# Kernel tuning notes

Hardware: AMD Instinct MI355X
Metric: run time of the kernel (lower is better)

The kernel has to match this reference:

```python
import jax, jax.numpy as jnp
import numpy as np


def _conv1x1(x, w, b):
    # x: [B, Cin, H, W], w: [Cout, Cin], b: [Cout]
    return jnp.einsum('bchw,oc->bohw', x, w) + b[None, :, None, None]


def setup_inputs() -> dict:
    key = jax.random.key(0)
    ks = jax.random.split(key, 9)
    B, C, H, W = 32, 512, 32, 32
    Cout, dn = 512, 512
    s_in = 1.0 / np.sqrt(C)
    s_out = 1.0 / np.sqrt(Cout)
    return {
        'x': jax.random.normal(ks[0], (B, C, H, W), jnp.float32),
        'wA': jax.random.uniform(ks[1], (Cout, C), jnp.float32, -s_in, s_in),
        'bA': jax.random.uniform(ks[2], (Cout,), jnp.float32, -s_in, s_in),
        'wB': jax.random.uniform(ks[3], (dn, C), jnp.float32, -s_in, s_in),
        'bB': jax.random.uniform(ks[4], (dn,), jnp.float32, -s_in, s_in),
        'wV': jax.random.uniform(ks[5], (dn, C), jnp.float32, -s_in, s_in),
        'bV': jax.random.uniform(ks[6], (dn,), jnp.float32, -s_in, s_in),
        'wR': jax.random.uniform(ks[7], (Cout, Cout), jnp.float32, -s_out, s_out),
        'bR': jax.random.uniform(ks[8], (Cout,), jnp.float32, -s_out, s_out),
    }


def reference(x, wA, bA, wB, bB, wV, bV, wR, bR):
    Bsz, C, H, W = x.shape
    Cout = wA.shape[0]
    A = _conv1x1(x, wA, bA).reshape(Bsz, Cout, H * W)          # [B, Cout, N]
    Bm = _conv1x1(x, wB, bB).reshape(Bsz, wB.shape[0], H * W)  # [B, dn, N]
    Vm = _conv1x1(x, wV, bV).reshape(Bsz, wV.shape[0], H * W)  # [B, dn, N]
    attn_maps = jax.nn.softmax(Bm, axis=-1)                    # softmax over spatial
    attn_vectors = jax.nn.softmax(Vm, axis=-1)                 # softmax over spatial
    glob_desc = jnp.einsum('bcn,bdn->bcd', A, attn_maps)       # [B, Cout, dn]
    Z = jnp.einsum('bcd,bdn->bcn', glob_desc, attn_vectors)    # [B, Cout, N]
    Z = Z.reshape(Bsz, Cout, H, W)
    Z = _conv1x1(Z, wR, bR)
    return Z
```

## Files before the change

### kernel.cpp

```cpp
#include <hip/hip_runtime.h>
#include <stdint.h>

typedef unsigned short u16;
typedef __bf16  bf16x8 __attribute__((ext_vector_type(8)));
typedef float   f32x4  __attribute__((ext_vector_type(4)));

__device__ __forceinline__ u16 f2bf(float f) {
    union { float f; unsigned u; } c; c.f = f;
    unsigned r = c.u + 0x7fffu + ((c.u >> 16) & 1u);
    return (u16)(r >> 16);
}
__device__ __forceinline__ float bf2f(u16 b) {
    union { unsigned u; float f; } c; c.u = ((unsigned)b) << 16; return c.f;
}

__device__ __forceinline__ void g2l16(const u16* g, u16* l) {
    __builtin_amdgcn_global_load_lds(
        (__attribute__((address_space(1))) void*)(uintptr_t)g,
        (__attribute__((address_space(3))) void*)(uint32_t)(uintptr_t)l,
        16, 0, 0);
}

template <int TM, bool HAS_BIAS, bool OUT_F32, bool EPI>
__device__ __forceinline__ void gemm_core(
    const u16* __restrict__ Ab, const u16* __restrict__ Bb, void* __restrict__ C,
    const float* __restrict__ bias, int N, int K, long cbase, int m0, int n0,
    const float* __restrict__ svec, const float* __restrict__ wRbA)
{
    constexpr int MI = TM / 32;
    constexpr int NA = TM / 32;
    __shared__ __align__(16) u16 As[TM * 64];
    __shared__ __align__(16) u16 Bs[128 * 64];

    const int t = threadIdx.x;
    const int w = t >> 6, lane = t & 63;
    const int wr = w >> 1, wc = w & 1;

    f32x4 acc[MI][4];
    const f32x4 zero = {0.f, 0.f, 0.f, 0.f};
#pragma unroll
    for (int i = 0; i < MI; ++i)
#pragma unroll
        for (int j = 0; j < 4; ++j) acc[i][j] = zero;

    int  aslot[NA]; long aoff[NA];
#pragma unroll
    for (int i = 0; i < NA; ++i) {
        const int s   = i * 256 + t;
        const int row = s >> 3;
        const int col = ((s & 7) ^ (row & 7)) * 8;
        aslot[i] = s * 8;
        aoff[i]  = (long)(m0 + row) * K + col;
    }
    int  bslot[4]; long boff[4];
#pragma unroll
    for (int i = 0; i < 4; ++i) {
        const int s   = i * 256 + t;
        const int row = s >> 3;
        const int col = ((s & 7) ^ (row & 7)) * 8;
        bslot[i] = s * 8;
        boff[i]  = (long)(n0 + row) * K + col;
    }

    const int fr = lane & 15;
    const int q  = lane >> 4;
    const int o0 = ((q ^ (fr & 7)) * 8);
    const u16* fa = &As[(wr * (TM / 2) + fr) * 64];
    const u16* fb = &Bs[(wc * 64 + fr) * 64];

    for (int k0 = 0; k0 < K; k0 += 64) {
#pragma unroll
        for (int i = 0; i < NA; ++i) g2l16(Ab + aoff[i] + k0, &As[aslot[i]]);
#pragma unroll
        for (int i = 0; i < 4; ++i)  g2l16(Bb + boff[i] + k0, &Bs[bslot[i]]);
        __syncthreads();

#pragma unroll
        for (int kh = 0; kh < 2; ++kh) {
            const int o = o0 ^ (kh * 32);
            bf16x8 af[MI], bv[4];
#pragma unroll
            for (int mi = 0; mi < MI; ++mi) af[mi] = *(const bf16x8*)(fa + mi * 1024 + o);
#pragma unroll
            for (int ni = 0; ni < 4; ++ni)  bv[ni] = *(const bf16x8*)(fb + ni * 1024 + o);
#pragma unroll
            for (int mi = 0; mi < MI; ++mi)
#pragma unroll
                for (int ni = 0; ni < 4; ++ni)
                    acc[mi][ni] = __builtin_amdgcn_mfma_f32_16x16x32_bf16(
                        af[mi], bv[ni], acc[mi][ni], 0, 0, 0);
        }
        __syncthreads();
    }

    const int ccol  = n0 + wc * 64 + fr;
    const int crow0 = m0 + wr * (TM / 2) + (lane >> 4) * 4;
    float se[4];
    if (EPI) {
#pragma unroll
        for (int ni = 0; ni < 4; ++ni) se[ni] = svec[ccol + ni * 16];
    }
#pragma unroll
    for (int mi = 0; mi < MI; ++mi) {
#pragma unroll
        for (int r = 0; r < 4; ++r) {
            const int row = crow0 + mi * 16 + r;
            float add = HAS_BIAS ? bias[row] : 0.f;
            float rk  = EPI ? wRbA[row] : 0.f;
#pragma unroll
            for (int ni = 0; ni < 4; ++ni) {
                float v = acc[mi][ni][r] + add;
                if (EPI) v += rk * se[ni];
                const long idx = cbase + (long)row * N + ccol + ni * 16;
                if (OUT_F32) ((float*)C)[idx] = v;
                else         ((u16*)C)[idx]   = f2bf(v);
            }
        }
    }
}

template <int TM, bool HAS_BIAS, bool OUT_F32>
__global__ __launch_bounds__(256) void gemm_nt(
    const u16* __restrict__ A, const u16* __restrict__ B, void* __restrict__ C,
    const float* __restrict__ bias, int N, int K, long sA, long sB, long sC)
{
    const int bz = blockIdx.z;
    gemm_core<TM, HAS_BIAS, OUT_F32, false>(
        A + (long)bz * sA, B + (long)bz * sB, C, bias, N, K,
        (long)bz * sC, blockIdx.y * TM, blockIdx.x * 128, nullptr, nullptr);
}

template <int TM, bool HAS_BIAS, bool OUT_F32, bool EPI>
__global__ __launch_bounds__(256) void gemm_nt_swz(
    const u16* __restrict__ A, const u16* __restrict__ B, void* __restrict__ C,
    const float* __restrict__ bias, int N, int K, long sA, long sB, long sC,
    int bxn, int bpb, const float* __restrict__ s_all,
    const float* __restrict__ wRbA)
{
    const int blk  = blockIdx.x;
    const int xcd  = blk & 7;
    const int slot = blk >> 3;
    const int b    = xcd + 8 * (slot / bpb);
    const int wi   = slot % bpb;
    const int bx   = wi % bxn;
    const int by   = wi / bxn;
    gemm_core<TM, HAS_BIAS, OUT_F32, EPI>(
        A + (long)b * sA, B + (long)b * sB, C, bias, N, K,
        (long)b * sC, by * TM, bx * 128,
        EPI ? s_all + (long)b * 1024 : nullptr, wRbA);
}

__global__ __launch_bounds__(256) void cast_transpose_x(
    const float* __restrict__ in, u16* __restrict__ out)
{
    __shared__ u16 tile[64][68];
    const int bz = blockIdx.z;
    const float* ip = in  + (long)bz * (512 * 1024);
    u16*         op = out + (long)bz * (1024 * 512);
    const int c0 = blockIdx.x * 64;
    const int r0 = blockIdx.y * 64;
    const int tx = threadIdx.x & 15;
    const int ty = threadIdx.x >> 4;
#pragma unroll
    for (int p = 0; p < 4; ++p) {
        const int row = ty + 16 * p;
        float4 v = *(const float4*)(ip + (long)(r0 + row) * 1024 + c0 + 4 * tx);
        ushort4 o;
        o.x = f2bf(v.x); o.y = f2bf(v.y); o.z = f2bf(v.z); o.w = f2bf(v.w);
        *(ushort4*)&tile[row][4 * tx] = o;
    }
    __syncthreads();
#pragma unroll
    for (int p = 0; p < 4; ++p) {
        const int orow = ty + 16 * p;
        ushort4 o;
        o.x = tile[4 * tx + 0][orow];
        o.y = tile[4 * tx + 1][orow];
        o.z = tile[4 * tx + 2][orow];
        o.w = tile[4 * tx + 3][orow];
        *(ushort4*)&op[(long)(c0 + orow) * 512 + r0 + 4 * tx] = o;
    }
}

__global__ __launch_bounds__(256) void transpose_colsum(
    const u16* __restrict__ in, u16* __restrict__ out, float* __restrict__ s,
    long sIn, long sOut)
{
    __shared__ u16 tile[64][68];
    const int bz = blockIdx.z;
    const u16* ip = in  + (long)bz * sIn;
    u16*       op = out + (long)bz * sOut;
    const int c0 = blockIdx.x * 64;
    const int r0 = blockIdx.y * 64;
    const int t  = threadIdx.x;
    const int tx = t & 15;
    const int ty = t >> 4;
#pragma unroll
    for (int p = 0; p < 4; ++p) {
        const int row = ty + 16 * p;
        ushort4 v = *(const ushort4*)(ip + (long)(r0 + row) * 1024 + c0 + 4 * tx);
        *(ushort4*)&tile[row][4 * tx] = v;
    }
    __syncthreads();
#pragma unroll
    for (int p = 0; p < 4; ++p) {
        const int orow = ty + 16 * p;
        ushort4 o;
        o.x = tile[4 * tx + 0][orow];
        o.y = tile[4 * tx + 1][orow];
        o.z = tile[4 * tx + 2][orow];
        o.w = tile[4 * tx + 3][orow];
        *(ushort4*)&op[(long)(c0 + orow) * 512 + r0 + 4 * tx] = o;
    }
    if (t < 64) {
        float a = 0.f;
#pragma unroll 8
        for (int d = 0; d < 64; ++d) a += bf2f(tile[d][t]);
        atomicAdd(&s[(long)bz * 1024 + c0 + t], a);
    }
}

__global__ __launch_bounds__(256) void cast_weights(
    const float* __restrict__ wA, const float* __restrict__ wB,
    const float* __restrict__ wV, const float* __restrict__ wR,
    const float* __restrict__ bB, const float* __restrict__ bV,
    u16* __restrict__ Wcat, u16* __restrict__ wRb, u16* __restrict__ wAtb,
    float* __restrict__ bcat)
{
    const int tid = blockIdx.x * 256 + threadIdx.x;
    if (tid < 262144) {
        Wcat[262144 + tid] = f2bf(wB[tid]);
    } else if (tid < 524288) {
        Wcat[262144 + tid] = f2bf(wV[tid - 262144]);
    } else if (tid < 786432) {
        wRb[tid - 524288] = f2bf(wR[tid - 524288]);
    } else if (tid < 1048576) {
        const int i = tid - 786432;
        wAtb[(i & 511) * 512 + (i >> 9)] = f2bf(wA[i]);
    } else if (tid < 1048576 + 1536) {
        const int j = tid - 1048576;
        bcat[j] = (j < 512) ? 0.f : (j < 1024) ? bB[j - 512] : bV[j - 1024];
    }
}

__global__ __launch_bounds__(256) void compute_wrba(
    const float* __restrict__ wR, const float* __restrict__ bA,
    float* __restrict__ wRbA)
{
    const int o    = blockIdx.x * 4 + (threadIdx.x >> 6);
    const int lane = threadIdx.x & 63;
    float a = 0.f;
#pragma unroll
    for (int c = lane; c < 512; c += 64) a += wR[o * 512 + c] * bA[c];
#pragma unroll
    for (int off = 32; off > 0; off >>= 1) a += __shfl_down(a, off);
    if (lane == 0) wRbA[o] = a;
}

__global__ __launch_bounds__(256) void softmax_rows(u16* __restrict__ Y)
{
    u16* row = Y + (long)blockIdx.y * (1536 * 1024) + (long)(512 + blockIdx.x) * 1024;
    const int t = threadIdx.x;
    ushort4 u = ((const ushort4*)row)[t];
    float v0 = bf2f(u.x), v1 = bf2f(u.y), v2 = bf2f(u.z), v3 = bf2f(u.w);

    float m = fmaxf(fmaxf(v0, v1), fmaxf(v2, v3));
#pragma unroll
    for (int off = 32; off > 0; off >>= 1) m = fmaxf(m, __shfl_down(m, off));

    __shared__ float smax[4];
    __shared__ float ssum[4];
    const int w = t >> 6, lane = t & 63;
    if (lane == 0) smax[w] = m;
    __syncthreads();
    m = fmaxf(fmaxf(smax[0], smax[1]), fmaxf(smax[2], smax[3]));

    float e0 = __expf(v0 - m), e1 = __expf(v1 - m);
    float e2 = __expf(v2 - m), e3 = __expf(v3 - m);
    float s = e0 + e1 + e2 + e3;
#pragma unroll
    for (int off = 32; off > 0; off >>= 1) s += __shfl_down(s, off);
    if (lane == 0) ssum[w] = s;
    __syncthreads();
    const float inv = 1.0f / (ssum[0] + ssum[1] + ssum[2] + ssum[3]);

    ushort4 o;
    o.x = f2bf(e0 * inv); o.y = f2bf(e1 * inv);
    o.z = f2bf(e2 * inv); o.w = f2bf(e3 * inv);
    ((ushort4*)row)[t] = o;
}

extern "C" void kernel_launch(void* const* d_in, const int* in_sizes, int n_in,
                              void* d_out, int out_size, void* d_ws, size_t ws_size,
                              hipStream_t stream)
{
    (void)in_sizes; (void)n_in; (void)out_size; (void)ws_size;
    const float* x  = (const float*)d_in[0];
    const float* wA = (const float*)d_in[1];
    const float* bA = (const float*)d_in[2];
    const float* wB = (const float*)d_in[3];
    const float* bB = (const float*)d_in[4];
    const float* wV = (const float*)d_in[5];
    const float* bV = (const float*)d_in[6];
    const float* wR = (const float*)d_in[7];
    const float* bR = (const float*)d_in[8];
    float* out = (float*)d_out;

    const int B = 32;
    const long sY = (long)1536 * 1024;

    char* p = (char*)d_ws;
    u16*   Y    = (u16*)p;   p += (long)B * sY * 2;
    u16*   H    = (u16*)p;   p += (long)B * 512 * 512 * 2;
    u16*   Wcat = (u16*)p;   p += (long)1536 * 512 * 2;
    u16*   wRb  = (u16*)p;   p += (long)512 * 512 * 2;
    u16*   wAtb = (u16*)p;   p += (long)512 * 512 * 2;
    float* bcat = (float*)p; p += 1536 * 4;
    float* svec = (float*)p; p += (long)B * 1024 * 4;
    float* wRbA = (float*)p; p += 512 * 4;

    u16* Xt = (u16*)d_out;
    u16* Vt = Y;

    cast_transpose_x<<<dim3(16, 8, B), 256, 0, stream>>>(x, Xt);
    cast_weights<<<dim3(4103), 256, 0, stream>>>(wA, wB, wV, wR, bB, bV,
                                                 Wcat, wRb, wAtb, bcat);
    compute_wrba<<<dim3(128), 256, 0, stream>>>(wR, bA, wRbA);
    hipMemsetAsync(svec, 0, (long)B * 1024 * 4, stream);

    gemm_nt<128, false, false><<<dim3(4, 4, 1), 256, 0, stream>>>(
        wRb, wAtb, Wcat, nullptr, 512, 512, 0, 0, 0);

    gemm_nt<128, true, false><<<dim3(8, 12, B), 256, 0, stream>>>(
        Wcat, Xt, Y, bcat, 1024, 512, 0, (long)1024 * 512, sY);

    softmax_rows<<<dim3(1024, B), 256, 0, stream>>>(Y);

    gemm_nt_swz<128, false, false, false><<<dim3(512), 256, 0, stream>>>(
        Y, Y + (long)512 * 1024, H, nullptr, 512, 1024,
        sY, sY, (long)512 * 512, 4, 16, nullptr, nullptr);

    transpose_colsum<<<dim3(16, 8, B), 256, 0, stream>>>(
        Y + (long)1024 * 1024, Vt, svec, sY, sY);

    gemm_nt_swz<128, true, true, true><<<dim3(1024), 256, 0, stream>>>(
        H, Vt, out, bR, 1024, 512, (long)512 * 512, sY, (long)512 * 1024,
        8, 32, svec, wRbA);
}
```

Before: 309.0 us.

## Replace projection GEMM with 256x256-tile, 512-thread, 4-stage pipelined kernel

```diff
diff --git a/kernel.cpp b/kernel.cpp
--- a/kernel.cpp
+++ b/kernel.cpp
@@ -148,6 +148,130 @@
         A + (long)b * sA, B + (long)b * sB, C, bias, N, K,
         (long)b * sC, by * TM, bx * 128,
         EPI ? s_all + (long)b * 1024 : nullptr, wRbA);
+}
+
+__global__ __launch_bounds__(512) void gemm2_y(
+    const u16* __restrict__ A,
+    const u16* __restrict__ B,
+    u16* __restrict__ C,
+    const float* __restrict__ bias)
+{
+    constexpr int K    = 512;
+    constexpr int NT   = K / 32;
+    constexpr int AREG = 256 * 32;
+    constexpr int BUFQ = 2 * AREG;
+    __shared__ __align__(16) u16 lds[4 * BUFQ];
+
+    const int bz = blockIdx.z;
+    const int m0 = blockIdx.y * 256;
+    const int n0 = blockIdx.x * 256;
+    const u16* Ab = A;
+    const u16* Bb = B + (long)bz * (1024 * 512);
+    u16*       Cb = C + (long)bz * ((long)1536 * 1024);
+
+    const int t    = threadIdx.x;
+    const int w    = t >> 6, lane = t & 63;
+    const int wr   = w >> 2, wc = w & 3;
+    const int fr   = lane & 15, q = lane >> 4;
+
+    int  aslot[2]; long agoff[2], bgoff[2];
+#pragma unroll
+    for (int i = 0; i < 2; ++i) {
+        const int ci  = i * 512 + t;
+        const int row = ci >> 2;
+        const int gc  = (ci & 3) ^ ((row >> 1) & 3);
+        aslot[i] = ci * 8;
+        agoff[i] = (long)(m0 + row) * K + gc * 8;
+        bgoff[i] = (long)(n0 + row) * K + gc * 8;
+    }
+
+    const int rchunk = (q ^ ((fr >> 1) & 3)) * 8;
+    const int abase  = (wr * 128 + fr) * 32 + rchunk;
+    const int bbase  = (wc * 64  + fr) * 32 + rchunk;
+
+    f32x4 acc[8][4];
+    const f32x4 zero = {0.f, 0.f, 0.f, 0.f};
+#pragma unroll
+    for (int i = 0; i < 8; ++i)
+#pragma unroll
+        for (int j = 0; j < 4; ++j) acc[i][j] = zero;
+
+#pragma unroll
+    for (int i = 0; i < 2; ++i) g2l16(Ab + agoff[i],        &lds[aslot[i]]);
+#pragma unroll
+    for (int i = 0; i < 2; ++i) g2l16(Bb + bgoff[i],        &lds[AREG + aslot[i]]);
+#pragma unroll
+    for (int i = 0; i < 2; ++i) g2l16(Ab + agoff[i] + 32,   &lds[BUFQ + aslot[i]]);
+#pragma unroll
+    for (int i = 0; i < 2; ++i) g2l16(Bb + bgoff[i] + 32,   &lds[BUFQ + AREG + aslot[i]]);
+    asm volatile("s_waitcnt vmcnt(4)" ::: "memory");
+    __builtin_amdgcn_s_barrier();
+
+#pragma unroll 1
+    for (int kt = 0; kt < NT; ++kt) {
+        const u16* Abuf = &lds[(kt & 3) * BUFQ];
+        const u16* Bbuf = Abuf + AREG;
+        u16* dst = &lds[((kt + 2) & 3) * BUFQ];
+        const long kg = (long)(kt + 2) * 32;
+        const bool stg = (kt + 2 < NT);
+
+        bf16x8 av[4], bv[4];
+#pragma unroll
+        for (int mi = 0; mi < 4; ++mi) av[mi] = *(const bf16x8*)(Abuf + abase + mi * 512);
+#pragma unroll
+        for (int ni = 0; ni < 4; ++ni) bv[ni] = *(const bf16x8*)(Bbuf + bbase + ni * 512);
+        if (stg) {
+#pragma unroll
+            for (int i = 0; i < 2; ++i) g2l16(Ab + agoff[i] + kg, dst + aslot[i]);
+        }
+        __builtin_amdgcn_s_barrier();
+        __builtin_amdgcn_s_setprio(1);
+#pragma unroll
+        for (int mi = 0; mi < 4; ++mi)
+#pragma unroll
+            for (int ni = 0; ni < 4; ++ni)
+                acc[mi][ni] = __builtin_amdgcn_mfma_f32_16x16x32_bf16(
+                    av[mi], bv[ni], acc[mi][ni], 0, 0, 0);
+        __builtin_amdgcn_s_setprio(0);
+        __builtin_amdgcn_s_barrier();
+
+        bf16x8 av2[4];
+#pragma unroll
+        for (int mi = 0; mi < 4; ++mi) av2[mi] = *(const bf16x8*)(Abuf + abase + (mi + 4) * 512);
+        if (stg) {
+#pragma unroll
+            for (int i = 0; i < 2; ++i) g2l16(Bb + bgoff[i] + kg, dst + AREG + aslot[i]);
+        }
+        __builtin_amdgcn_s_barrier();
+        __builtin_amdgcn_s_setprio(1);
+#pragma unroll
+        for (int mi = 0; mi < 4; ++mi)
+#pragma unroll
+            for (int ni = 0; ni < 4; ++ni)
+                acc[mi + 4][ni] = __builtin_amdgcn_mfma_f32_16x16x32_bf16(
+                    av2[mi], bv[ni], acc[mi + 4][ni], 0, 0, 0);
+        __builtin_amdgcn_s_setprio(0);
+
+        if (kt + 1 < NT) {
+            if (kt + 2 < NT) asm volatile("s_waitcnt vmcnt(4)" ::: "memory");
+            else             asm volatile("s_waitcnt vmcnt(0)" ::: "memory");
+            __builtin_amdgcn_s_barrier();
+        }
+    }
+
+    const int ccol  = n0 + wc * 64 + fr;
+    const int crow0 = m0 + wr * 128 + q * 4;
+#pragma unroll
+    for (int mi = 0; mi < 8; ++mi) {
+#pragma unroll
+        for (int r = 0; r < 4; ++r) {
+            const int row = crow0 + mi * 16 + r;
+            const float add = bias[row];
+#pragma unroll
+            for (int ni = 0; ni < 4; ++ni)
+                Cb[(long)row * 1024 + ccol + ni * 16] = f2bf(acc[mi][ni][r] + add);
+        }
+    }
 }
 
 __global__ __launch_bounds__(256) void cast_transpose_x(
@@ -331,8 +455,7 @@
     gemm_nt<128, false, false><<<dim3(4, 4, 1), 256, 0, stream>>>(
         wRb, wAtb, Wcat, nullptr, 512, 512, 0, 0, 0);
 
-    gemm_nt<128, true, false><<<dim3(8, 12, B), 256, 0, stream>>>(
-        Wcat, Xt, Y, bcat, 1024, 512, 0, (long)1024 * 512, sY);
+    gemm2_y<<<dim3(4, 6, B), 512, 0, stream>>>(Wcat, Xt, Y, bcat);
 
     softmax_rows<<<dim3(1024, B), 256, 0, stream>>>(Y);
 
```

After: 311.5 us. About the same (+0.8%).
